# Performance work log

Hardware: AMD Instinct MI355X
Metric: run time of the kernel (lower is better)

## Reference

```python
import jax, jax.numpy as jnp
import numpy as np

N = 20000          # num nodes
DEG = 8            # directed avg degree before symmetrization
IN_C, HID, OUT_C, K = 128, 32, 16, 2


def _build_graph(n, deg, seed=0):
    """Build symmetric 1-hop A1 (no self loops) and exact 2-hop A2 edge lists,
    with D^{-1/2} A D^{-1/2} normalized values (mirrors _prepare_prop)."""
    rng = np.random.default_rng(seed)
    e = n * deg
    row = rng.integers(0, n, e)
    col = rng.integers(0, n, e)
    r = np.concatenate([row, col])
    c = np.concatenate([col, row])
    m = r != c
    keys1 = np.unique(r[m].astype(np.int64) * n + c[m])  # A1 = indicator(A - I)
    r1 = (keys1 // n).astype(np.int64)
    c1 = (keys1 % n).astype(np.int64)
    # exact 2-hop: nonzeros of A1@A1, minus A1 and diagonal
    degs = np.bincount(r1, minlength=n)
    indptr = np.concatenate([np.zeros(1, np.int64), np.cumsum(degs)])
    counts = degs[c1]                       # per edge (u,v): deg(v)
    cum = np.cumsum(counts)
    total = int(cum[-1])
    offs = np.arange(total) - np.repeat(cum - counts, counts)
    dst2 = c1[np.repeat(indptr[c1], counts) + offs]
    src2 = np.repeat(r1, counts)
    keys2 = np.unique(src2 * n + dst2)
    diag = np.arange(n, dtype=np.int64) * (n + 1)
    keys2 = np.setdiff1d(keys2, np.concatenate([keys1, diag]), assume_unique=True)
    r2 = (keys2 // n).astype(np.int64)
    c2 = (keys2 % n).astype(np.int64)

    def norm(rr, cc):  # D^{-1/2} A D^{-1/2} on binary symmetric adjacency
        d = np.bincount(rr, minlength=n).astype(np.float64)
        dis = np.where(d > 0, 1.0 / np.sqrt(np.maximum(d, 1.0)), 0.0)
        return (dis[rr] * dis[cc]).astype(np.float32)

    return r1, c1, norm(r1, c1), r2, c2, norm(r2, c2)


def setup_inputs() -> dict:
    key = jax.random.key(0)
    k1, k2, k3 = jax.random.split(key, 3)
    x = jax.random.normal(k1, (N, IN_C), dtype=jnp.float32)
    # xavier_uniform for the two dense weights
    ae = float(np.sqrt(6.0 / (IN_C + HID)))
    cdim = (2 ** (K + 1) - 1) * HID  # 224
    ac = float(np.sqrt(6.0 / (cdim + OUT_C)))
    w_embed = jax.random.uniform(k2, (IN_C, HID), jnp.float32, -ae, ae)
    w_classify = jax.random.uniform(k3, (cdim, OUT_C), jnp.float32, -ac, ac)
    r1, c1, v1, r2, c2, v2 = _build_graph(N, DEG)
    return {
        "x": x, "w_embed": w_embed, "w_classify": w_classify,
        "a1_row": jnp.asarray(r1), "a1_col": jnp.asarray(c1), "a1_val": jnp.asarray(v1),
        "a2_row": jnp.asarray(r2), "a2_col": jnp.asarray(c2), "a2_val": jnp.asarray(v2),
    }


def _spmm(row, col, val, x, n):
    # sparse @ dense: gather source rows, scale, scatter-add into dest rows
    return jax.ops.segment_sum(x[col] * val[:, None], row, num_segments=n)


def reference(x, w_embed, w_classify, a1_row, a1_col, a1_val, a2_row, a2_col, a2_val):
    n = x.shape[0]
    rs = [jax.nn.relu(x @ w_embed)]  # [N, HID]
    for _ in range(K):
        r = rs[-1]
        r1 = _spmm(a1_row, a1_col, a1_val, r, n)
        r2 = _spmm(a2_row, a2_col, a2_val, r, n)
        rs.append(jax.nn.relu(jnp.concatenate([r1, r2], axis=1)))
    r_final = jnp.concatenate(rs, axis=1)  # [N, 7*HID]; dropout is identity in eval
    return r_final @ w_classify            # [N, OUT_C]
```

## Files before the change

### kernel.cpp

```cpp
#include <hip/hip_runtime.h>

typedef unsigned int uint;
typedef unsigned short ushort;

#define IN_C 128
#define HID  32

__device__ __forceinline__ uint f2h2(float a, float b) {
    _Float16 ha = (_Float16)a, hb = (_Float16)b;
    unsigned short ua = __builtin_bit_cast(unsigned short, ha);
    unsigned short ub = __builtin_bit_cast(unsigned short, hb);
    return (uint)ua | ((uint)ub << 16);
}
__device__ __forceinline__ void fma_lo(float& acc, uint pk, float v) {
    asm("v_fma_mix_f32 %0, %1, %2, %0 op_sel:[0,0,0] op_sel_hi:[1,0,0]"
        : "+v"(acc) : "v"(pk), "v"(v));
}
__device__ __forceinline__ void fma_hi(float& acc, uint pk, float v) {
    asm("v_fma_mix_f32 %0, %1, %2, %0 op_sel:[1,0,0] op_sel_hi:[1,0,0]"
        : "+v"(acc) : "v"(pk), "v"(v));
}

typedef const __attribute__((address_space(1))) void* gas1_t;
typedef __attribute__((address_space(3))) void*       las3_t;
__device__ __forceinline__ void glds16(const void* g, void* l) {
    __builtin_amdgcn_global_load_lds((gas1_t)g, (las3_t)l, 16, 0, 0);
}

__global__ void prep_kernel(const float* __restrict__ x,
                            const float* __restrict__ w,
                            ushort* __restrict__ r0,
                            const int* __restrict__ a1r, int E1, int* __restrict__ ip1,
                            const int* __restrict__ a2r, int E2, int* __restrict__ ip2,
                            const int* __restrict__ a2c, const float* __restrict__ a2v,
                            float* __restrict__ dummy,
                            int n, int nbE, int nbI, int nbT) {
    __shared__ float wl[IN_C * HID];
    const int tid = threadIdx.x;
    if (blockIdx.x < nbE) {
        for (int i = tid; i < IN_C * HID; i += blockDim.x) wl[i] = w[i];
        __syncthreads();
        const int row = blockIdx.x * 16 + tid / 16;
        const int h0  = (tid % 16) * 2;
        if (row >= n) return;
        const float4* xr = (const float4*)(x + (size_t)row * IN_C);
        float a0 = 0.f, a1 = 0.f;
#pragma unroll
        for (int k4 = 0; k4 < IN_C / 4; ++k4) {
            float4 xv = xr[k4];
            a0 += xv.x * wl[(4*k4+0)*HID + h0];  a1 += xv.x * wl[(4*k4+0)*HID + h0+1];
            a0 += xv.y * wl[(4*k4+1)*HID + h0];  a1 += xv.y * wl[(4*k4+1)*HID + h0+1];
            a0 += xv.z * wl[(4*k4+2)*HID + h0];  a1 += xv.z * wl[(4*k4+2)*HID + h0+1];
            a0 += xv.w * wl[(4*k4+3)*HID + h0];  a1 += xv.w * wl[(4*k4+3)*HID + h0+1];
        }
        uint p = f2h2(fmaxf(a0, 0.f), fmaxf(a1, 0.f));
        ((uint*)r0)[(size_t)row * 16 + (tid % 16)] = p;
    } else if (blockIdx.x < nbE + nbI) {
        const int i = (blockIdx.x - nbE) * 256 + tid;
        if (i > n) return;
        int lo = 0, hi = E1;
        while (lo < hi) { int m = (lo + hi) >> 1; if (a1r[m] < i) lo = m + 1; else hi = m; }
        ip1[i] = lo;
        lo = 0; hi = E2;
        while (lo < hi) { int m = (lo + hi) >> 1; if (a2r[m] < i) lo = m + 1; else hi = m; }
        ip2[i] = lo;
    } else {
        const int t = (blockIdx.x - nbE - nbI) * 256 + tid;
        const int stride = nbT * 256;
        const int total4 = E2 / 4;
        const float4* c4 = (const float4*)a2c;
        const float4* v4 = (const float4*)a2v;
        float s = 0.f;
        for (int i = t; i < total4; i += stride) {
            float4 u = c4[i], v = v4[i];
            s += u.x + u.y + u.z + u.w + v.x + v.y + v.z + v.w;
        }
        if (s == 123.456f) dummy[0] = s;
    }
}

template <int C, int ROWSL>
__global__ __launch_bounds__(256) void spmm_level(
        const int* __restrict__ ip1, const int* __restrict__ col1,
        const float* __restrict__ val1, int E1,
        const int* __restrict__ ip2, const int* __restrict__ col2,
        const float* __restrict__ val2, int E2,
        const ushort* __restrict__ xin, ushort* __restrict__ out,
        int n, int nbH) {
    constexpr int L = C / 8;
    __shared__ __align__(16) int   scol[4][256];
    __shared__ __align__(16) float sval[4][256];

    const int lane = threadIdx.x & 63;
    const int wave = threadIdx.x >> 6;
    (void)E1;

    int bid = blockIdx.x;
    if (bid < nbH) {
        constexpr int W = 64 / L;
        const int fl  = lane % L;
        const int way = lane / L;
        const uint flo = (uint)fl * 16u;

        auto gat = [&](uint c) -> uint4 {
            return *(const uint4*)((const char*)xin + (c * (uint)(2 * C) + flo));
        };
        float acc[8];
#pragma unroll
        for (int j = 0; j < 8; ++j) acc[j] = 0.f;
        auto fmadd = [&](const uint4& u, float v) {
            fma_lo(acc[0], u.x, v); fma_hi(acc[1], u.x, v);
            fma_lo(acc[2], u.y, v); fma_hi(acc[3], u.y, v);
            fma_lo(acc[4], u.z, v); fma_hi(acc[5], u.z, v);
            fma_lo(acc[6], u.w, v); fma_hi(acc[7], u.w, v);
        };

        const int row = bid * 4 + wave;
        if (row >= n) return;
        const int s = ip2[row];
        const int e = ip2[row + 1];

        int sv = (s + 3) & ~3; if (sv > e) sv = e;
        for (int idx = s + way; idx < sv; idx += W)
            fmadd(gat((uint)col2[idx]), val2[idx]);

        const int lastA = (E2 - 4) & ~3;
        int*   myc = &scol[wave][0];
        float* myv = &sval[wave][0];

        for (int base = sv; base < e; base += 256) {
            const int cnt = (e - base < 256) ? (e - base) : 256;
            int so = base + lane * 4; if (so > lastA) so = lastA;
            glds16(col2 + so, myc);
            glds16(val2 + so, myv);
            asm volatile("s_waitcnt vmcnt(0)" ::: "memory");
            __builtin_amdgcn_sched_barrier(0);
            const int nb = cnt / (4 * W);
            for (int b = 0; b < nb; ++b) {
                const int o = (b * W + way) * 4;
                const int4   cc = *(const int4*)  (myc + o);
                const float4 vv = *(const float4*)(myv + o);
                const uint4 g0 = gat((uint)cc.x), g1 = gat((uint)cc.y),
                            g2 = gat((uint)cc.z), g3 = gat((uint)cc.w);
                fmadd(g0, vv.x); fmadd(g1, vv.y);
                fmadd(g2, vv.z); fmadd(g3, vv.w);
            }
            for (int k = nb * 4 * W + way; k < cnt; k += W)
                fmadd(gat((uint)myc[k]), myv[k]);
        }

#pragma unroll
        for (int m = L; m < 64; m <<= 1)
#pragma unroll
            for (int j = 0; j < 8; ++j) acc[j] += __shfl_xor(acc[j], m, 64);

        if (way == 0) {
            uint4 p;
            p.x = f2h2(fmaxf(acc[0], 0.f), fmaxf(acc[1], 0.f));
            p.y = f2h2(fmaxf(acc[2], 0.f), fmaxf(acc[3], 0.f));
            p.z = f2h2(fmaxf(acc[4], 0.f), fmaxf(acc[5], 0.f));
            p.w = f2h2(fmaxf(acc[6], 0.f), fmaxf(acc[7], 0.f));
            *(uint4*)(out + (size_t)row * (2 * C) + C + fl * 8) = p;
        }
    } else {
        bid -= nbH;
        constexpr int SUBL = 64 / ROWSL;
        constexpr int WL   = SUBL / L;
        const int sub = lane / SUBL;
        const int li  = lane % SUBL;
        const int fl  = li % L;
        const int way = li / L;
        const uint flo = (uint)fl * 16u;

        auto gat = [&](uint c) -> uint4 {
            return *(const uint4*)((const char*)xin + (c * (uint)(2 * C) + flo));
        };
        float acc[8];
#pragma unroll
        for (int j = 0; j < 8; ++j) acc[j] = 0.f;
        auto fmadd = [&](const uint4& u, float v) {
            fma_lo(acc[0], u.x, v); fma_hi(acc[1], u.x, v);
            fma_lo(acc[2], u.y, v); fma_hi(acc[3], u.y, v);
            fma_lo(acc[4], u.z, v); fma_hi(acc[5], u.z, v);
            fma_lo(acc[6], u.w, v); fma_hi(acc[7], u.w, v);
        };

        const int row = (bid * 4 + wave) * ROWSL + sub;
        if (row >= n) return;
        const int s = ip1[row];
        const int e = ip1[row + 1];
        int idx0 = s + way;
        if (idx0 < e) {
            int c0 = col1[idx0]; float v0 = val1[idx0];
            int idx1 = idx0 + WL;
            int c1 = 0; float v1 = 0.f;
            if (idx1 < e) { c1 = col1[idx1]; v1 = val1[idx1]; }
            uint4 g0 = gat((uint)c0);
            while (true) {
                int idx2 = idx1 + WL;
                int c2 = 0; float v2 = 0.f;
                if (idx2 < e) { c2 = col1[idx2]; v2 = val1[idx2]; }
                uint4 g1 = gat((uint)c1);
                fmadd(g0, v0);
                if (idx1 >= e) break;
                g0 = g1; c1 = c2; v0 = v1; v1 = v2;
                idx1 = idx2;
            }
        }
#pragma unroll
        for (int m = L; m < SUBL; m <<= 1)
#pragma unroll
            for (int j = 0; j < 8; ++j) acc[j] += __shfl_xor(acc[j], m, 64);
        if (way == 0) {
            uint4 p;
            p.x = f2h2(fmaxf(acc[0], 0.f), fmaxf(acc[1], 0.f));
            p.y = f2h2(fmaxf(acc[2], 0.f), fmaxf(acc[3], 0.f));
            p.z = f2h2(fmaxf(acc[4], 0.f), fmaxf(acc[5], 0.f));
            p.w = f2h2(fmaxf(acc[6], 0.f), fmaxf(acc[7], 0.f));
            *(uint4*)(out + (size_t)row * (2 * C) + fl * 8) = p;
        }
    }
}

#define CDIM 224
#define OUT_C 16
__global__ void classify_kernel(const ushort* __restrict__ r0,
                                const ushort* __restrict__ r1,
                                const ushort* __restrict__ r2,
                                const float* __restrict__ w,
                                float* __restrict__ out, int n) {
    __shared__ float wl[CDIM * OUT_C];
    const int tid = threadIdx.x;
    for (int i = tid; i < CDIM * OUT_C; i += blockDim.x) wl[i] = w[i];
    __syncthreads();
    const int row = blockIdx.x * 16 + tid / 16;
    const int o   = tid % 16;
    if (row >= n) return;
    float acc = 0.f;

    const uint4* a = (const uint4*)(r0 + (size_t)row * 32);
#pragma unroll
    for (int q = 0; q < 4; ++q) {
        uint4 u = a[q]; int j = q * 8;
        fma_lo(acc, u.x, wl[(j+0)*OUT_C + o]);  fma_hi(acc, u.x, wl[(j+1)*OUT_C + o]);
        fma_lo(acc, u.y, wl[(j+2)*OUT_C + o]);  fma_hi(acc, u.y, wl[(j+3)*OUT_C + o]);
        fma_lo(acc, u.z, wl[(j+4)*OUT_C + o]);  fma_hi(acc, u.z, wl[(j+5)*OUT_C + o]);
        fma_lo(acc, u.w, wl[(j+6)*OUT_C + o]);  fma_hi(acc, u.w, wl[(j+7)*OUT_C + o]);
    }
    const uint4* b = (const uint4*)(r1 + (size_t)row * 64);
#pragma unroll
    for (int q = 0; q < 8; ++q) {
        uint4 u = b[q]; int j = 32 + q * 8;
        fma_lo(acc, u.x, wl[(j+0)*OUT_C + o]);  fma_hi(acc, u.x, wl[(j+1)*OUT_C + o]);
        fma_lo(acc, u.y, wl[(j+2)*OUT_C + o]);  fma_hi(acc, u.y, wl[(j+3)*OUT_C + o]);
        fma_lo(acc, u.z, wl[(j+4)*OUT_C + o]);  fma_hi(acc, u.z, wl[(j+5)*OUT_C + o]);
        fma_lo(acc, u.w, wl[(j+6)*OUT_C + o]);  fma_hi(acc, u.w, wl[(j+7)*OUT_C + o]);
    }
    const uint4* c = (const uint4*)(r2 + (size_t)row * 128);
#pragma unroll
    for (int q = 0; q < 16; ++q) {
        uint4 u = c[q]; int j = 96 + q * 8;
        fma_lo(acc, u.x, wl[(j+0)*OUT_C + o]);  fma_hi(acc, u.x, wl[(j+1)*OUT_C + o]);
        fma_lo(acc, u.y, wl[(j+2)*OUT_C + o]);  fma_hi(acc, u.y, wl[(j+3)*OUT_C + o]);
        fma_lo(acc, u.z, wl[(j+4)*OUT_C + o]);  fma_hi(acc, u.z, wl[(j+5)*OUT_C + o]);
        fma_lo(acc, u.w, wl[(j+6)*OUT_C + o]);  fma_hi(acc, u.w, wl[(j+7)*OUT_C + o]);
    }
    out[(size_t)row * OUT_C + o] = acc;
}

extern "C" void kernel_launch(void* const* d_in, const int* in_sizes, int n_in,
                              void* d_out, int out_size, void* d_ws, size_t ws_size,
                              hipStream_t stream) {
    const float* x   = (const float*)d_in[0];
    const float* we  = (const float*)d_in[1];
    const float* wc  = (const float*)d_in[2];
    const int*   a1r = (const int*)  d_in[3];
    const int*   a1c = (const int*)  d_in[4];
    const float* a1v = (const float*)d_in[5];
    const int*   a2r = (const int*)  d_in[6];
    const int*   a2c = (const int*)  d_in[7];
    const float* a2v = (const float*)d_in[8];
    float* out = (float*)d_out;

    const int E1 = in_sizes[3];
    const int E2 = in_sizes[6];
    const int n  = in_sizes[0] / IN_C;

    ushort* r0 = (ushort*)d_ws;
    ushort* r1 = r0 + (size_t)n * 32;
    ushort* r2 = r1 + (size_t)n * 64;
    int*   ip1 = (int*)(r2 + (size_t)n * 128);
    int*   ip2 = ip1 + (n + 1);
    float* dummy = (float*)(ip2 + (n + 2));

    {
        const int nbE = (n + 15) / 16;
        const int nbI = (n + 1 + 255) / 256;
        const int nbT = 512;
        prep_kernel<<<nbE + nbI + nbT, 256, 0, stream>>>(
            x, we, r0, a1r, E1, ip1, a2r, E2, ip2, a2c, a2v, dummy,
            n, nbE, nbI, nbT);
    }

    {
        const int nbH = (n + 3) / 4;
        const int nbL = (n + 7) / 8;
        spmm_level<32, 2><<<nbH + nbL, 256, 0, stream>>>(
            ip1, a1c, a1v, E1, ip2, a2c, a2v, E2, r0, r1, n, nbH);
    }
    {
        const int nbH = (n + 3) / 4;
        const int nbL = (n + 3) / 4;
        spmm_level<64, 1><<<nbH + nbL, 256, 0, stream>>>(
            ip1, a1c, a1v, E1, ip2, a2c, a2v, E2, r1, r2, n, nbH);
    }

    classify_kernel<<<(n + 15) / 16, 256, 0, stream>>>(r0, r1, r2, wc, out, n);
}
```

Measured before the change: 205.4 us.

## Double-buffer 2-hop index staging and process two rows per wave

In the 2-hop branch of the SpMM kernel, each wave now handles two consecutive rows. Their edge chunks are streamed through a double-buffered LDS staging area, so the next chunk's column and value loads are issued while the current chunk is being consumed (waitcnt vmcnt(2) instead of a full drain). Tail edges past the aligned end of the array are handled separately so the clamped vector loads stay in bounds. This halves the number of 2-hop blocks and hides index-load latency. In exchange it doubles accumulator registers and LDS use, and adds more branching per chunk.

```diff
diff --git a/kernel.cpp b/kernel.cpp
--- a/kernel.cpp
+++ b/kernel.cpp
@@ -88,8 +88,8 @@
         const ushort* __restrict__ xin, ushort* __restrict__ out,
         int n, int nbH) {
     constexpr int L = C / 8;
-    __shared__ __align__(16) int   scol[4][256];
-    __shared__ __align__(16) float sval[4][256];
+    __shared__ __align__(16) int   scol[4][2][256];
+    __shared__ __align__(16) float sval[4][2][256];
 
     const int lane = threadIdx.x & 63;
     const int wave = threadIdx.x >> 6;
@@ -105,63 +105,109 @@
         auto gat = [&](uint c) -> uint4 {
             return *(const uint4*)((const char*)xin + (c * (uint)(2 * C) + flo));
         };
-        float acc[8];
-#pragma unroll
-        for (int j = 0; j < 8; ++j) acc[j] = 0.f;
-        auto fmadd = [&](const uint4& u, float v) {
-            fma_lo(acc[0], u.x, v); fma_hi(acc[1], u.x, v);
-            fma_lo(acc[2], u.y, v); fma_hi(acc[3], u.y, v);
-            fma_lo(acc[4], u.z, v); fma_hi(acc[5], u.z, v);
-            fma_lo(acc[6], u.w, v); fma_hi(acc[7], u.w, v);
-        };
-
-        const int row = bid * 4 + wave;
-        if (row >= n) return;
-        const int s = ip2[row];
-        const int e = ip2[row + 1];
-
-        int sv = (s + 3) & ~3; if (sv > e) sv = e;
-        for (int idx = s + way; idx < sv; idx += W)
-            fmadd(gat((uint)col2[idx]), val2[idx]);
-
-        const int lastA = (E2 - 4) & ~3;
-        int*   myc = &scol[wave][0];
-        float* myv = &sval[wave][0];
-
-        for (int base = sv; base < e; base += 256) {
-            const int cnt = (e - base < 256) ? (e - base) : 256;
-            int so = base + lane * 4; if (so > lastA) so = lastA;
-            glds16(col2 + so, myc);
-            glds16(val2 + so, myv);
-            asm volatile("s_waitcnt vmcnt(0)" ::: "memory");
-            __builtin_amdgcn_sched_barrier(0);
+        float accA[8], accB[8];
+#pragma unroll
+        for (int j = 0; j < 8; ++j) { accA[j] = 0.f; accB[j] = 0.f; }
+        auto fmadd = [&](float (&ac)[8], const uint4& u, float v) {
+            fma_lo(ac[0], u.x, v); fma_hi(ac[1], u.x, v);
+            fma_lo(ac[2], u.y, v); fma_hi(ac[3], u.y, v);
+            fma_lo(ac[4], u.z, v); fma_hi(ac[5], u.z, v);
+            fma_lo(ac[6], u.w, v); fma_hi(ac[7], u.w, v);
+        };
+
+        const int rowA = (bid * 4 + wave) * 2;
+        const int rowB = rowA + 1;
+        if (rowA >= n) return;
+        const bool hasB = (rowB < n);
+
+        const int sA = ip2[rowA];
+        const int eA = ip2[rowA + 1];
+        const int sB = eA;
+        const int eB = hasB ? ip2[rowB + 1] : eA;
+
+        const int cut      = E2 & ~3;
+        const int clampOff = (E2 - 4) & ~3;
+
+        int svA = (sA + 3) & ~3; if (svA > eA) svA = eA;
+        int svB = (sB + 3) & ~3; if (svB > eB) svB = eB;
+        for (int idx = sA + way; idx < svA; idx += W)
+            fmadd(accA, gat((uint)col2[idx]), val2[idx]);
+        for (int idx = sB + way; idx < svB; idx += W)
+            fmadd(accB, gat((uint)col2[idx]), val2[idx]);
+        int eeA = eA, eeB = eB;
+        if (eeA > cut) {
+            int st = (svA > cut) ? svA : cut;
+            for (int idx = st + way; idx < eeA; idx += W)
+                fmadd(accA, gat((uint)col2[idx]), val2[idx]);
+            eeA = st;
+        }
+        if (eeB > cut) {
+            int st = (svB > cut) ? svB : cut;
+            for (int idx = st + way; idx < eeB; idx += W)
+                fmadd(accB, gat((uint)col2[idx]), val2[idx]);
+            eeB = st;
+        }
+
+        const int ncA = (eeA - svA + 255) >> 8;
+        const int ncB = (eeB - svB + 255) >> 8;
+        const int nc  = ncA + ncB;
+
+        auto chunkBase = [&](int j) -> int {
+            int jj = (j < nc) ? j : (nc - 1);
+            return (jj < ncA) ? (svA + (jj << 8)) : (svB + ((jj - ncA) << 8));
+        };
+        auto stage = [&](int buf, int base) {
+            int so = base + lane * 4; if (so > clampOff) so = clampOff;
+            glds16(col2 + so, &scol[wave][buf][0]);
+            glds16(val2 + so, &sval[wave][buf][0]);
+        };
+        auto consume = [&](float (&ac)[8], const int* mc, const float* mv, int cnt) {
             const int nb = cnt / (4 * W);
             for (int b = 0; b < nb; ++b) {
                 const int o = (b * W + way) * 4;
-                const int4   cc = *(const int4*)  (myc + o);
-                const float4 vv = *(const float4*)(myv + o);
+                const int4   cc = *(const int4*)  (mc + o);
+                const float4 vv = *(const float4*)(mv + o);
                 const uint4 g0 = gat((uint)cc.x), g1 = gat((uint)cc.y),
                             g2 = gat((uint)cc.z), g3 = gat((uint)cc.w);
-                fmadd(g0, vv.x); fmadd(g1, vv.y);
-                fmadd(g2, vv.z); fmadd(g3, vv.w);
+                fmadd(ac, g0, vv.x); fmadd(ac, g1, vv.y);
+                fmadd(ac, g2, vv.z); fmadd(ac, g3, vv.w);
             }
             for (int k = nb * 4 * W + way; k < cnt; k += W)
-                fmadd(gat((uint)myc[k]), myv[k]);
-        }
-
-#pragma unroll
-        for (int m = L; m < 64; m <<= 1)
-#pragma unroll
-            for (int j = 0; j < 8; ++j) acc[j] += __shfl_xor(acc[j], m, 64);
-
-        if (way == 0) {
-            uint4 p;
-            p.x = f2h2(fmaxf(acc[0], 0.f), fmaxf(acc[1], 0.f));
-            p.y = f2h2(fmaxf(acc[2], 0.f), fmaxf(acc[3], 0.f));
-            p.z = f2h2(fmaxf(acc[4], 0.f), fmaxf(acc[5], 0.f));
-            p.w = f2h2(fmaxf(acc[6], 0.f), fmaxf(acc[7], 0.f));
-            *(uint4*)(out + (size_t)row * (2 * C) + C + fl * 8) = p;
-        }
+                fmadd(ac, gat((uint)mc[k]), mv[k]);
+        };
+
+        if (nc > 0) {
+            stage(0, chunkBase(0));
+            for (int j = 0; j < nc; ++j) {
+                stage((j + 1) & 1, chunkBase(j + 1));
+                asm volatile("s_waitcnt vmcnt(2)" ::: "memory");
+                const bool isA = (j < ncA);
+                const int base = isA ? (svA + (j << 8)) : (svB + ((j - ncA) << 8));
+                const int end  = isA ? eeA : eeB;
+                int cnt = end - base; if (cnt > 256) cnt = 256;
+                const int*   mc = &scol[wave][j & 1][0];
+                const float* mv = &sval[wave][j & 1][0];
+                if (isA) consume(accA, mc, mv, cnt);
+                else     consume(accB, mc, mv, cnt);
+            }
+        }
+
+        auto redstore = [&](float (&ac)[8], int row) {
+#pragma unroll
+            for (int m = L; m < 64; m <<= 1)
+#pragma unroll
+                for (int j = 0; j < 8; ++j) ac[j] += __shfl_xor(ac[j], m, 64);
+            if (way == 0) {
+                uint4 p;
+                p.x = f2h2(fmaxf(ac[0], 0.f), fmaxf(ac[1], 0.f));
+                p.y = f2h2(fmaxf(ac[2], 0.f), fmaxf(ac[3], 0.f));
+                p.z = f2h2(fmaxf(ac[4], 0.f), fmaxf(ac[5], 0.f));
+                p.w = f2h2(fmaxf(ac[6], 0.f), fmaxf(ac[7], 0.f));
+                *(uint4*)(out + (size_t)row * (2 * C) + C + fl * 8) = p;
+            }
+        };
+        redstore(accA, rowA);
+        if (hasB) redstore(accB, rowB);
     } else {
         bid -= nbH;
         constexpr int SUBL = 64 / ROWSL;
@@ -303,13 +349,13 @@
     }
 
     {
-        const int nbH = (n + 3) / 4;
+        const int nbH = (n + 7) / 8;
         const int nbL = (n + 7) / 8;
         spmm_level<32, 2><<<nbH + nbL, 256, 0, stream>>>(
             ip1, a1c, a1v, E1, ip2, a2c, a2v, E2, r0, r1, n, nbH);
     }
     {
-        const int nbH = (n + 3) / 4;
+        const int nbH = (n + 7) / 8;
         const int nbL = (n + 3) / 4;
         spmm_level<64, 1><<<nbH + nbL, 256, 0, stream>>>(
             ip1, a1c, a1v, E1, ip2, a2c, a2v, E2, r1, r2, n, nbH);
```

After: 215.7 us. 5.0% more time.
